# Optimization experiments

Measured on AMD Instinct MI355X. Metric: run time of the kernel, lower is better.

Reference implementation:

```python
import jax, jax.numpy as jnp
import numpy as np

B, S, D_MODEL, HEADS = 2, 2048, 1024, 16
HEAD_DIM = D_MODEL // HEADS
NEG = -1.0e9


def setup_inputs() -> dict:
    key = jax.random.key(0)
    ks = jax.random.split(key, 7)
    query = jax.random.normal(ks[0], (B, S, D_MODEL), dtype=jnp.float32)
    k_in = jax.random.normal(ks[1], (B, S, D_MODEL), dtype=jnp.float32)
    value = jax.random.normal(ks[2], (B, S, D_MODEL), dtype=jnp.float32)
    # nn.Linear(d_model, d_model, bias=False) weights, torch layout [out, in]
    sc = 1.0 / np.sqrt(D_MODEL)
    Wq = jax.random.uniform(ks[3], (D_MODEL, D_MODEL), jnp.float32, -sc, sc)
    Wk = jax.random.uniform(ks[4], (D_MODEL, D_MODEL), jnp.float32, -sc, sc)
    Wv = jax.random.uniform(ks[5], (D_MODEL, D_MODEL), jnp.float32, -sc, sc)
    Wo = jax.random.uniform(ks[6], (D_MODEL, D_MODEL), jnp.float32, -sc, sc)
    # causal mask: 1 where attention allowed, 0 where masked
    mask = jnp.tril(jnp.ones((S, S), dtype=jnp.int32))[None, None]
    freqs_complex_form = jnp.zeros((1,), dtype=jnp.float32)  # unused by the module
    return {"query": query, "key": k_in, "value": value,
            "freqs_complex_form": freqs_complex_form, "mask": mask,
            "Wq": Wq, "Wk": Wk, "Wv": Wv, "Wo": Wo}


def reference(query, key, value, freqs_complex_form, mask, Wq, Wk, Wv, Wo):
    # QKV projections (torch Linear: y = x @ W.T)
    q = query @ Wq.T
    k = key @ Wk.T
    v = value @ Wv.T
    # [B, S, D] -> [B, H, S, Dh]
    q = q.reshape(B, S, HEADS, HEAD_DIM).transpose(0, 2, 1, 3)
    k = k.reshape(B, S, HEADS, HEAD_DIM).transpose(0, 2, 1, 3)
    v = v.reshape(B, S, HEADS, HEAD_DIM).transpose(0, 2, 1, 3)
    # scores [B, H, S, S]
    att = jnp.einsum('bhqd,bhkd->bhqk', q, k) / jnp.sqrt(jnp.float32(HEAD_DIM))
    att = jnp.where(mask == 0, NEG, att)
    att = jax.nn.softmax(att, axis=-1)
    # dropout is identity in eval / deterministic reference
    out = jnp.einsum('bhqk,bhkd->bhqd', att, v)
    out = out.transpose(0, 2, 1, 3).reshape(B, S, D_MODEL)
    return out @ Wo.T
```

## Files before the change

### kernel.cpp

```cpp
#include <hip/hip_runtime.h>

#define DM   1024
#define SEQ  2048
#define BATCH 2
#define NH   16
#define DHEAD 64
#define MTOT (BATCH*SEQ)
#define KVB  64
#define EOFF ((size_t)MTOT * DM)
#define NROW (BATCH * NH * SEQ)

typedef _Float16 half_t;
typedef _Float16 half4 __attribute__((ext_vector_type(4)));
typedef _Float16 half8 __attribute__((ext_vector_type(8)));
typedef float    floatx4 __attribute__((ext_vector_type(4)));

#define SCALE2 0.18033688f

__device__ __forceinline__ float fast_exp2(float x) {
  float r;
  asm volatile("v_exp_f32 %0, %1" : "=v"(r) : "v"(x));
  return r;
}

__device__ __forceinline__ void gload_lds16(const half_t* g, half_t* l) {
  __builtin_amdgcn_global_load_lds(
      (const __attribute__((address_space(1))) void*)g,
      (__attribute__((address_space(3))) void*)l, 16, 0, 0);
}

__global__ __launch_bounds__(256) void cvt_all(const float* __restrict__ q, const float* __restrict__ k,
                                               const float* __restrict__ v, const float* __restrict__ wq,
                                               const float* __restrict__ wk, const float* __restrict__ wv,
                                               const float* __restrict__ wo,
                                               half_t* __restrict__ dq, half_t* __restrict__ dk,
                                               half_t* __restrict__ dv, half_t* __restrict__ dwq,
                                               half_t* __restrict__ dwk, half_t* __restrict__ dwv,
                                               half_t* __restrict__ dwo) {
  const int y = blockIdx.y;
  const float* s; half_t* d; int n8;
  const int En8 = MTOT * DM / 8, Wn8 = DM * DM / 8;
  switch (y) {
    case 0: s = q;  d = dq;  n8 = En8; break;
    case 1: s = k;  d = dk;  n8 = En8; break;
    case 2: s = v;  d = dv;  n8 = En8; break;
    case 3: s = wq; d = dwq; n8 = Wn8; break;
    case 4: s = wk; d = dwk; n8 = Wn8; break;
    case 5: s = wv; d = dwv; n8 = Wn8; break;
    default: s = wo; d = dwo; n8 = Wn8; break;
  }
  int i = blockIdx.x * 256 + threadIdx.x;
  if (i >= n8) return;
  const float4* sp = reinterpret_cast<const float4*>(s);
  float4 u = sp[(size_t)i * 2], w = sp[(size_t)i * 2 + 1];
  half8 h;
  h[0] = (half_t)u.x; h[1] = (half_t)u.y; h[2] = (half_t)u.z; h[3] = (half_t)u.w;
  h[4] = (half_t)w.x; h[5] = (half_t)w.y; h[6] = (half_t)w.z; h[7] = (half_t)w.w;
  *reinterpret_cast<half8*>(d + (size_t)i * 8) = h;
}

__global__ __launch_bounds__(256) void gemm_qkv(const half_t* __restrict__ Xq,
                                                const half_t* __restrict__ Xk,
                                                const half_t* __restrict__ Xv,
                                                const half_t* __restrict__ Wq,
                                                const half_t* __restrict__ Wk,
                                                const half_t* __restrict__ Wv,
                                                half_t* __restrict__ Qb,
                                                half_t* __restrict__ Kb,
                                                half_t* __restrict__ Vb) {
  __shared__ half_t As[2][128 * 32];
  __shared__ half_t Bs[2][128 * 32];
  const int which = blockIdx.x >> 8;
  const int flat = blockIdx.x & 255;
  const half_t* Ag = (which == 0) ? Xq : (which == 1) ? Xk : Xv;
  const half_t* Bg = (which == 0) ? Wq : (which == 1) ? Wk : Wv;
  half_t* Cg       = (which == 0) ? Qb : (which == 1) ? Kb : Vb;
  const float esc  = (which == 0) ? SCALE2 : 1.0f;

  const int tid = threadIdx.x, lane = tid & 63, w = tid >> 6;
  const int lr = lane & 15, lg = lane >> 4;
  const int xcd = flat & 7, bi = flat >> 3;
  const int m0 = (xcd * 4 + (bi >> 3)) * 128;
  const int n0 = (bi & 7) * 128;
  const int wm = (w >> 1) * 64, wn = (w & 1) * 64;
  floatx4 acc[4][4] = {};

#define STAGE_QKV(BUF, K0)                                                    \
  {                                                                           \
    _Pragma("unroll")                                                         \
    for (int j = 0; j < 2; j++) {                                             \
      int id = tid + j * 256;                                                 \
      gload_lds16(Ag + (size_t)(m0 + (id >> 2)) * DM + (K0) + (id & 3) * 8,   \
                  &As[BUF][id * 8]);                                          \
      gload_lds16(Bg + (size_t)(n0 + (id >> 2)) * DM + (K0) + (id & 3) * 8,   \
                  &Bs[BUF][id * 8]);                                          \
    }                                                                         \
  }
#define COMP_QKV(BUF)                                                         \
  {                                                                           \
    half8 a[4], b[4];                                                         \
    _Pragma("unroll")                                                         \
    for (int i = 0; i < 4; i++)                                               \
      a[i] = *reinterpret_cast<half8*>(&As[BUF][(wm + i * 16 + lr) * 32 + lg * 8]); \
    _Pragma("unroll")                                                         \
    for (int j = 0; j < 4; j++)                                               \
      b[j] = *reinterpret_cast<half8*>(&Bs[BUF][(wn + j * 16 + lr) * 32 + lg * 8]); \
    _Pragma("unroll")                                                         \
    for (int i = 0; i < 4; i++)                                               \
      _Pragma("unroll")                                                       \
      for (int j = 0; j < 4; j++)                                             \
        acc[i][j] = __builtin_amdgcn_mfma_f32_16x16x32_f16(b[j], a[i], acc[i][j], 0, 0, 0); \
  }

  STAGE_QKV(0, 0);
  __syncthreads();
  int buf = 0;
#pragma unroll 1
  for (int t = 0; t < 31; t++) {
    STAGE_QKV(buf ^ 1, (t + 1) * 32);
    COMP_QKV(buf);
    __syncthreads();
    buf ^= 1;
  }
  COMP_QKV(buf);

#pragma unroll
  for (int i = 0; i < 4; i++) {
    const int m = m0 + wm + i * 16 + lr;
    const int b_ = m >> 11, s_ = m & 2047;
#pragma unroll
    for (int j = 0; j < 4; j++) {
      const int n = n0 + wn + j * 16 + lg * 4;
      const int h_ = n >> 6, d_ = n & 63;
      half4 o;
#pragma unroll
      for (int r = 0; r < 4; r++) o[r] = (half_t)(acc[i][j][r] * esc);
      *reinterpret_cast<half4*>(
          &Cg[(((size_t)b_ * NH + h_) * SEQ + s_) * DHEAD + d_]) = o;
    }
  }
#undef STAGE_QKV
#undef COMP_QKV
}

__global__ __launch_bounds__(256) void gemm_o(const half_t* __restrict__ Ag,
                                              const half_t* __restrict__ Bg,
                                              float* __restrict__ Cg) {
  __shared__ half_t As[2][128 * 32];
  __shared__ half_t Bs[2][64 * 32];
  const int tid = threadIdx.x, lane = tid & 63, w = tid >> 6;
  const int lr = lane & 15, lg = lane >> 4;
  const int flat = blockIdx.x;
  const int xcd = flat & 7, bi = flat >> 3;
  const int m0 = (xcd * 4 + (bi >> 4)) * 128;
  const int n0 = (bi & 15) * 64;
  const int wm = (w >> 1) * 64, wn = (w & 1) * 32;
  floatx4 acc[4][2] = {};

#define STAGE_O(BUF, K0)                                                      \
  {                                                                           \
    _Pragma("unroll")                                                         \
    for (int j = 0; j < 2; j++) {                                             \
      int id = tid + j * 256;                                                 \
      gload_lds16(Ag + (size_t)(m0 + (id >> 2)) * DM + (K0) + (id & 3) * 8,   \
                  &As[BUF][id * 8]);                                          \
    }                                                                         \
    gload_lds16(Bg + (size_t)(n0 + (tid >> 2)) * DM + (K0) + (tid & 3) * 8,   \
                &Bs[BUF][tid * 8]);                                           \
  }
#define COMP_O(BUF)                                                           \
  {                                                                           \
    half8 a[4], b[2];                                                         \
    _Pragma("unroll")                                                         \
    for (int i = 0; i < 4; i++)                                               \
      a[i] = *reinterpret_cast<half8*>(&As[BUF][(wm + i * 16 + lr) * 32 + lg * 8]); \
    _Pragma("unroll")                                                         \
    for (int j = 0; j < 2; j++)                                               \
      b[j] = *reinterpret_cast<half8*>(&Bs[BUF][(wn + j * 16 + lr) * 32 + lg * 8]); \
    _Pragma("unroll")                                                         \
    for (int i = 0; i < 4; i++)                                               \
      _Pragma("unroll")                                                       \
      for (int j = 0; j < 2; j++)                                             \
        acc[i][j] = __builtin_amdgcn_mfma_f32_16x16x32_f16(b[j], a[i], acc[i][j], 0, 0, 0); \
  }

  STAGE_O(0, 0);
  __syncthreads();
  int buf = 0;
#pragma unroll 1
  for (int t = 0; t < 31; t++) {
    STAGE_O(buf ^ 1, (t + 1) * 32);
    COMP_O(buf);
    __syncthreads();
    buf ^= 1;
  }
  COMP_O(buf);

#pragma unroll
  for (int i = 0; i < 4; i++) {
    const int m = m0 + wm + i * 16 + lr;
#pragma unroll
    for (int j = 0; j < 2; j++) {
      const int n = n0 + wn + j * 16 + lg * 4;
      floatx4 o = acc[i][j];
      *reinterpret_cast<floatx4*>(&Cg[(size_t)m * DM + n]) = o;
    }
  }
#undef STAGE_O
#undef COMP_O
}

__global__ __launch_bounds__(512) void attn_fwd(const half_t* __restrict__ Q,
                                                const half_t* __restrict__ K,
                                                const half_t* __restrict__ V,
                                                half_t* __restrict__ P,
                                                float* __restrict__ L) {
  __shared__ half_t Ks[64][72];
  __shared__ half_t Vt[80][72];
  __shared__ half_t Ps[8][16][72];
  const int tid = threadIdx.x, lane = tid & 63, w = tid >> 6;
  const int lr = lane & 15, lg = lane >> 4;

  const int flat = blockIdx.x;
  const int xcd = flat & 7, idx = flat >> 3;
  const int qblk = 15 - (idx >> 3);
  const int sub = idx & 7;
  const int combo = xcd * 4 + (sub >> 1);
  const int split = sub & 1;
  const int h = combo & 15, b = combo >> 4;

  const size_t bh = ((size_t)b * NH + h) * SEQ * DHEAD;
  const int q0 = qblk * 128 + w * 16;
  const int nt = 2 * (qblk + 1);
  const int h0 = qblk + 1;
  const int t0 = split ? h0 : 0;
  const int t1 = split ? nt : h0;

  for (int i2 = tid; i2 < 16 * 72; i2 += 512) {
    int d = i2 / 72, kv = i2 % 72;
    Vt[64 + d][kv] = (d == 0) ? (half_t)1.0f : (half_t)0.0f;
  }

  half8 qf[2];
#pragma unroll
  for (int ks = 0; ks < 2; ks++)
    qf[ks] = *reinterpret_cast<const half8*>(
        Q + bh + (size_t)(q0 + lr) * DHEAD + ks * 32 + lg * 8);

  floatx4 accO[5] = {};

  half8 kr, vr;
#define LOADT(t)                                                              \
  {                                                                           \
    const int kvb2 = (t) * KVB;                                               \
    kr = *reinterpret_cast<const half8*>(                                     \
        K + bh + (size_t)(kvb2 + (tid >> 3)) * DHEAD + (tid & 7) * 8);        \
    vr = *reinterpret_cast<const half8*>(                                     \
        V + bh + (size_t)(kvb2 + (tid & 63)) * DHEAD + (tid >> 6) * 8);       \
  }
#define WRITET()                                                              \
  {                                                                           \
    *reinterpret_cast<half8*>(&Ks[tid >> 3][(tid & 7) * 8]) = kr;             \
    int vrow = tid & 63, vcol = (tid >> 6) * 8;                               \
    _Pragma("unroll")                                                         \
    for (int e = 0; e < 8; e++) Vt[vcol + e][vrow] = vr[e];                   \
  }

  LOADT(t0);
  WRITET();
  __syncthreads();

#pragma unroll 1
  for (int t = t0; t < t1; t++) {
    const int kvbase = t * KVB;
    if (t + 1 < t1) LOADT(t + 1);
    if (kvbase <= q0 + 15) {
      const bool need_mask = (kvbase + KVB - 1) > q0;
      floatx4 s[4];
#pragma unroll
      for (int jt = 0; jt < 4; jt++) {
        floatx4 a0 = {};
#pragma unroll
        for (int ks = 0; ks < 2; ks++) {
          half8 ak = *reinterpret_cast<half8*>(&Ks[jt * 16 + lr][ks * 32 + lg * 8]);
          a0 = __builtin_amdgcn_mfma_f32_16x16x32_f16(ak, qf[ks], a0, 0, 0, 0);
        }
        s[jt] = a0;
      }
      const int qq = q0 + lr;
#pragma unroll
      for (int jt = 0; jt < 4; jt++) {
        half4 pk;
#pragma unroll
        for (int r = 0; r < 4; r++) {
          float pp = fast_exp2(s[jt][r]);
          if (need_mask) {
            int kv = kvbase + jt * 16 + lg * 4 + r;
            if (kv > qq) pp = 0.f;
          }
          pk[r] = (half_t)pp;
        }
        *reinterpret_cast<half4*>(&Ps[w][lr][jt * 16 + lg * 4]) = pk;
      }
      half8 ap0 = *reinterpret_cast<half8*>(&Ps[w][lr][lg * 8]);
      half8 ap1 = *reinterpret_cast<half8*>(&Ps[w][lr][32 + lg * 8]);
#pragma unroll
      for (int j = 0; j < 5; j++) {
        half8 bv0 = *reinterpret_cast<half8*>(&Vt[j * 16 + lr][lg * 8]);
        half8 bv1 = *reinterpret_cast<half8*>(&Vt[j * 16 + lr][32 + lg * 8]);
        accO[j] = __builtin_amdgcn_mfma_f32_16x16x32_f16(bv0, ap0, accO[j], 0, 0, 0);
        accO[j] = __builtin_amdgcn_mfma_f32_16x16x32_f16(bv1, ap1, accO[j], 0, 0, 0);
      }
    }
    if (t + 1 < t1) {
      __syncthreads();
      WRITET();
      __syncthreads();
    }
  }

  half_t* Pw = P + (size_t)split * EOFF;
  float*  Lw = L + (size_t)split * NROW;
  {
    const int q = q0 + lr;
    const size_t rowbase = bh + (size_t)q * DHEAD;
#pragma unroll
    for (int j = 0; j < 4; j++) {
      half4 o;
#pragma unroll
      for (int r = 0; r < 4; r++) o[r] = (half_t)accO[j][r];
      *reinterpret_cast<half4*>(&Pw[rowbase + j * 16 + lg * 4]) = o;
    }
    if (lg == 0)
      Lw[((size_t)b * NH + h) * SEQ + q] = accO[4][0];
  }
#undef LOADT
#undef WRITET
}

__global__ __launch_bounds__(256) void attn_combine(const half_t* __restrict__ P,
                                                    const float* __restrict__ L,
                                                    half_t* __restrict__ Ab) {
  size_t i = (size_t)blockIdx.x * 256 + threadIdx.x;
  half8 p0 = *reinterpret_cast<const half8*>(P + i * 8);
  half8 p1 = *reinterpret_cast<const half8*>(P + EOFF + i * 8);
  size_t row = i >> 3;
  float l = L[row] + L[NROW + row];
  float inv = 1.0f / l;
  int s_ = (int)(row % SEQ);
  int h_ = (int)((row / SEQ) % NH);
  int b_ = (int)(row / ((size_t)SEQ * NH));
  int d0 = (int)(i & 7) * 8;
  half8 o;
#pragma unroll
  for (int e = 0; e < 8; e++)
    o[e] = (half_t)(((float)p0[e] + (float)p1[e]) * inv);
  *reinterpret_cast<half8*>(Ab + ((size_t)b_ * SEQ + s_) * DM + h_ * DHEAD + d0) = o;
}

extern "C" void kernel_launch(void* const* d_in, const int* in_sizes, int n_in,
                              void* d_out, int out_size, void* d_ws, size_t ws_size,
                              hipStream_t stream) {
  const float* q_in = (const float*)d_in[0];
  const float* k_in = (const float*)d_in[1];
  const float* v_in = (const float*)d_in[2];
  const float* Wq   = (const float*)d_in[5];
  const float* Wk   = (const float*)d_in[6];
  const float* Wv   = (const float*)d_in[7];
  const float* Wo   = (const float*)d_in[8];

  const size_t E = EOFF;
  const size_t W = (size_t)DM * DM;
  half_t* ws  = (half_t*)d_ws;
  half_t* Xq  = ws;
  half_t* Xk  = ws + E;
  half_t* Xv  = ws + 2 * E;
  half_t* Wqh = ws + 3 * E;
  half_t* Wkh = Wqh + W;
  half_t* Wvh = Wkh + W;
  half_t* Woh = Wvh + W;
  half_t* Qb  = ws + 4 * E;
  half_t* Kb  = ws + 5 * E;
  half_t* Vb  = ws + 6 * E;
  half_t* Ab  = Xq;
  half_t* Pp  = Xk;
  float*  Lp  = (float*)Wqh;
  if (ws_size < 7 * E * sizeof(half_t)) return;

  cvt_all<<<dim3(2048, 7), 256, 0, stream>>>(q_in, k_in, v_in, Wq, Wk, Wv, Wo,
                                             Xq, Xk, Xv, Wqh, Wkh, Wvh, Woh);
  gemm_qkv<<<768, 256, 0, stream>>>(Xq, Xk, Xv, Wqh, Wkh, Wvh, Qb, Kb, Vb);
  attn_fwd<<<1024, 512, 0, stream>>>(Qb, Kb, Vb, Pp, Lp);
  attn_combine<<<2048, 256, 0, stream>>>(Pp, Lp, Ab);
  gemm_o<<<512, 256, 0, stream>>>(Ab, Woh, (float*)d_out);
}
```

Baseline: 129.3 us.

## Keep attention probabilities in registers and hoist GEMM staging address math

The attention kernel no longer stages the exponentiated scores through a per-wave shared-memory buffer. It packs them straight into MFMA operand registers and permutes the V reads from LDS so the k-index ordering lines up with the register layout of the score accumulators. The QKV and O projection GEMMs also precompute their per-thread global source pointers and LDS offsets once, instead of recomputing them at every stage. This removes an LDS write/read round trip per tile and some integer work, at the cost of narrower half4 V loads plus register shuffles.

```diff
diff --git a/kernel.cpp b/kernel.cpp
--- a/kernel.cpp
+++ b/kernel.cpp
@@ -85,15 +85,21 @@
   const int wm = (w >> 1) * 64, wn = (w & 1) * 64;
   floatx4 acc[4][4] = {};
 
+  const half_t* aSrc[2]; const half_t* bSrc[2]; int dstOff[2];
+#pragma unroll
+  for (int j = 0; j < 2; j++) {
+    int id = tid + j * 256;
+    aSrc[j] = Ag + (size_t)(m0 + (id >> 2)) * DM + (id & 3) * 8;
+    bSrc[j] = Bg + (size_t)(n0 + (id >> 2)) * DM + (id & 3) * 8;
+    dstOff[j] = id * 8;
+  }
+
 #define STAGE_QKV(BUF, K0)                                                    \
   {                                                                           \
     _Pragma("unroll")                                                         \
     for (int j = 0; j < 2; j++) {                                             \
-      int id = tid + j * 256;                                                 \
-      gload_lds16(Ag + (size_t)(m0 + (id >> 2)) * DM + (K0) + (id & 3) * 8,   \
-                  &As[BUF][id * 8]);                                          \
-      gload_lds16(Bg + (size_t)(n0 + (id >> 2)) * DM + (K0) + (id & 3) * 8,   \
-                  &Bs[BUF][id * 8]);                                          \
+      gload_lds16(aSrc[j] + (K0), &As[BUF][dstOff[j]]);                       \
+      gload_lds16(bSrc[j] + (K0), &Bs[BUF][dstOff[j]]);                       \
     }                                                                         \
   }
 #define COMP_QKV(BUF)                                                         \
@@ -157,16 +163,21 @@
   const int wm = (w >> 1) * 64, wn = (w & 1) * 32;
   floatx4 acc[4][2] = {};
 
+  const half_t* aSrc[2]; const half_t* bSrc; int dstOff[2];
+#pragma unroll
+  for (int j = 0; j < 2; j++) {
+    int id = tid + j * 256;
+    aSrc[j] = Ag + (size_t)(m0 + (id >> 2)) * DM + (id & 3) * 8;
+    dstOff[j] = id * 8;
+  }
+  bSrc = Bg + (size_t)(n0 + (tid >> 2)) * DM + (tid & 3) * 8;
+
 #define STAGE_O(BUF, K0)                                                      \
   {                                                                           \
     _Pragma("unroll")                                                         \
-    for (int j = 0; j < 2; j++) {                                             \
-      int id = tid + j * 256;                                                 \
-      gload_lds16(Ag + (size_t)(m0 + (id >> 2)) * DM + (K0) + (id & 3) * 8,   \
-                  &As[BUF][id * 8]);                                          \
-    }                                                                         \
-    gload_lds16(Bg + (size_t)(n0 + (tid >> 2)) * DM + (K0) + (tid & 3) * 8,   \
-                &Bs[BUF][tid * 8]);                                           \
+    for (int j = 0; j < 2; j++)                                               \
+      gload_lds16(aSrc[j] + (K0), &As[BUF][dstOff[j]]);                       \
+    gload_lds16(bSrc + (K0), &Bs[BUF][tid * 8]);                              \
   }
 #define COMP_O(BUF)                                                           \
   {                                                                           \
@@ -217,7 +228,6 @@
                                                 float* __restrict__ L) {
   __shared__ half_t Ks[64][72];
   __shared__ half_t Vt[80][72];
-  __shared__ half_t Ps[8][16][72];
   const int tid = threadIdx.x, lane = tid & 63, w = tid >> 6;
   const int lr = lane & 15, lg = lane >> 4;
 
@@ -289,8 +299,7 @@
       }
       const int qq = q0 + lr;
 #pragma unroll
-      for (int jt = 0; jt < 4; jt++) {
-        half4 pk;
+      for (int jt = 0; jt < 4; jt++)
 #pragma unroll
         for (int r = 0; r < 4; r++) {
           float pp = fast_exp2(s[jt][r]);
@@ -298,18 +307,28 @@
             int kv = kvbase + jt * 16 + lg * 4 + r;
             if (kv > qq) pp = 0.f;
           }
-          pk[r] = (half_t)pp;
+          s[jt][r] = pp;
         }
-        *reinterpret_cast<half4*>(&Ps[w][lr][jt * 16 + lg * 4]) = pk;
+      half8 pb[2];
+#pragma unroll
+      for (int ks = 0; ks < 2; ks++) {
+#pragma unroll
+        for (int e = 0; e < 4; e++) {
+          pb[ks][e]     = (half_t)s[2 * ks][e];
+          pb[ks][4 + e] = (half_t)s[2 * ks + 1][e];
+        }
       }
-      half8 ap0 = *reinterpret_cast<half8*>(&Ps[w][lr][lg * 8]);
-      half8 ap1 = *reinterpret_cast<half8*>(&Ps[w][lr][32 + lg * 8]);
 #pragma unroll
       for (int j = 0; j < 5; j++) {
-        half8 bv0 = *reinterpret_cast<half8*>(&Vt[j * 16 + lr][lg * 8]);
-        half8 bv1 = *reinterpret_cast<half8*>(&Vt[j * 16 + lr][32 + lg * 8]);
-        accO[j] = __builtin_amdgcn_mfma_f32_16x16x32_f16(bv0, ap0, accO[j], 0, 0, 0);
-        accO[j] = __builtin_amdgcn_mfma_f32_16x16x32_f16(bv1, ap1, accO[j], 0, 0, 0);
+#pragma unroll
+        for (int ks = 0; ks < 2; ks++) {
+          half4 x = *reinterpret_cast<half4*>(&Vt[j * 16 + lr][ks * 32 + lg * 4]);
+          half4 y = *reinterpret_cast<half4*>(&Vt[j * 16 + lr][ks * 32 + 16 + lg * 4]);
+          half8 av;
+          av[0] = x[0]; av[1] = x[1]; av[2] = x[2]; av[3] = x[3];
+          av[4] = y[0]; av[5] = y[1]; av[6] = y[2]; av[7] = y[3];
+          accO[j] = __builtin_amdgcn_mfma_f32_16x16x32_f16(av, pb[ks], accO[j], 0, 0, 0);
+        }
       }
     }
     if (t + 1 < t1) {
```

After: 129.2 us. Within noise of the previous version (-0.0%).
